# Kernel optimization log

Hardware: AMD Instinct MI355X
Metric: run time of the kernel (lower is better)

Reference implementation:

```python
import jax, jax.numpy as jnp
import numpy as np

N_NODES = 50000
N_EDGES = 600000
D_IN = 128
HID = 128
N_LAYERS = 4
N_OUT = 8
BN_EPS = 1e-5


def setup_inputs() -> dict:
    key = jax.random.key(0)
    ks = jax.random.split(key, 12)
    x = jax.random.normal(ks[0], (N_NODES, D_IN), dtype=jnp.float32)
    edge_index = jax.random.randint(ks[1], (2, N_EDGES), 0, N_NODES, dtype=jnp.int64)
    s = 1.0 / np.sqrt(HID)
    # per-layer GIN MLP params, stacked over layers (d_in == hidden so shapes match)
    W1 = jax.random.uniform(ks[2], (N_LAYERS, HID, HID), jnp.float32, -s, s)
    b1 = jax.random.uniform(ks[3], (N_LAYERS, HID), jnp.float32, -s, s)
    W2 = jax.random.uniform(ks[4], (N_LAYERS, HID, HID), jnp.float32, -s, s)
    b2 = jax.random.uniform(ks[5], (N_LAYERS, HID), jnp.float32, -s, s)
    gamma = jnp.ones((N_LAYERS, HID), jnp.float32)
    beta = jnp.zeros((N_LAYERS, HID), jnp.float32)
    s1 = 1.0 / np.sqrt(N_LAYERS * HID)
    lin1_W = jax.random.uniform(ks[6], (N_LAYERS * HID, HID), jnp.float32, -s1, s1)
    lin1_b = jax.random.uniform(ks[7], (HID,), jnp.float32, -s1, s1)
    lin2_W = jax.random.uniform(ks[8], (HID, N_OUT), jnp.float32, -s, s)
    lin2_b = jax.random.uniform(ks[9], (N_OUT,), jnp.float32, -s, s)
    return dict(x=x, edge_index=edge_index, W1=W1, b1=b1, W2=W2, b2=b2,
                gamma=gamma, beta=beta, lin1_W=lin1_W, lin1_b=lin1_b,
                lin2_W=lin2_W, lin2_b=lin2_b)


def _gin_layer(x, src, dst, W1, b1, W2, b2, g, bt):
    # GINConv, eps=0: h_i = MLP(x_i + sum_{j in N(i)} x_j)
    agg = jax.ops.segment_sum(x[src], dst, num_segments=N_NODES)  # [N, d]
    h = x + agg
    h = jax.nn.relu(h @ W1 + b1)
    h = jax.nn.relu(h @ W2 + b2)
    # BatchNorm1d (training-mode stats, biased variance)
    mean = jnp.mean(h, axis=0)
    var = jnp.var(h, axis=0)
    return (h - mean) * jax.lax.rsqrt(var + BN_EPS) * g + bt


def reference(x, edge_index, W1, b1, W2, b2, gamma, beta,
              lin1_W, lin1_b, lin2_W, lin2_b):
    src, dst = edge_index[0], edge_index[1]
    xs = []
    h = x
    for l in range(N_LAYERS):
        h = _gin_layer(h, src, dst, W1[l], b1[l], W2[l], b2[l], gamma[l], beta[l])
        xs.append(h)
    jk = jnp.concatenate(xs, axis=-1)          # JumpingKnowledge 'cat' -> [N, L*HID]
    out = jax.nn.relu(jk @ lin1_W + lin1_b)    # dropout is identity at inference
    out = out @ lin2_W + lin2_b                # [N, N_OUT]
    return out
```

## Files before the change

### kernel.cpp

```cpp
#include <hip/hip_runtime.h>

#define NNODES 50000
#define NEDGES 600000
#define HID 128
#define NLAYERS 4
#define NOUT 8
#define BN_EPS 1e-5f
#define NBLK 196
#define NPBLK 3125

typedef short short8 __attribute__((ext_vector_type(8)));
typedef float f32x4 __attribute__((ext_vector_type(4)));

__device__ inline unsigned short f2bf(float f) {
  unsigned u = __float_as_uint(f);
  unsigned r = ((u >> 16) & 1u) + 0x7fffu;
  return (unsigned short)((u + r) >> 16);
}
__device__ inline float bflo(unsigned w) { return __uint_as_float(w << 16); }
__device__ inline float bfhi(unsigned w) { return __uint_as_float(w & 0xffff0000u); }


__global__ void detect64_k(const int* __restrict__ ei, int* __restrict__ flag) {
  __shared__ int anynz;
  if (threadIdx.x == 0) anynz = 0;
  __syncthreads();
  int acc = 0;
  for (int i = threadIdx.x; i < 4096; i += 256) {
    int p = i * 146;
    acc |= ei[2 * p + 1];
  }
  if (acc != 0) anynz = 1;
  __syncthreads();
  if (threadIdx.x == 0) *flag = (anynz == 0) ? 1 : 0;
}

__global__ void cvt_bf_k(const float* __restrict__ src, unsigned short* __restrict__ dst,
                         int n4) {
  int i = blockIdx.x * 256 + threadIdx.x;
  if (i >= n4) return;
  float4 v = ((const float4*)src)[i];
  ushort4 o;
  o.x = f2bf(v.x);
  o.y = f2bf(v.y);
  o.z = f2bf(v.z);
  o.w = f2bf(v.w);
  ((ushort4*)dst)[i] = o;
}


__global__ void zero_deg_k(int* __restrict__ deg) {
  int i = blockIdx.x * 256 + threadIdx.x;
  if (i < NNODES + 1) deg[i] = 0;
}

__global__ void hist_k(const int* __restrict__ ei, const int* __restrict__ flag,
                       int* __restrict__ deg) {
  int e = blockIdx.x * 256 + threadIdx.x;
  if (e >= NEDGES) return;
  int d = (*flag) ? ei[2 * NEDGES + 2 * e] : ei[NEDGES + e];
  atomicAdd(&deg[d], 1);
}

__global__ void blocksum_k(const int* __restrict__ deg, int* __restrict__ bsum) {
  int t = threadIdx.x;
  int i = blockIdx.x * 256 + t;
  __shared__ int sh[256];
  sh[t] = (i < NNODES) ? deg[i] : 0;
  __syncthreads();
  for (int s = 128; s > 0; s >>= 1) {
    if (t < s) sh[t] += sh[t + s];
    __syncthreads();
  }
  if (t == 0) bsum[blockIdx.x] = sh[0];
}

__global__ void scanb_k(const int* __restrict__ bsum, int* __restrict__ boff) {
  __shared__ int sh[256];
  int t = threadIdx.x;
  sh[t] = (t < NBLK) ? bsum[t] : 0;
  __syncthreads();
  for (int d = 1; d < 256; d <<= 1) {
    int v = (t >= d) ? sh[t - d] : 0;
    __syncthreads();
    sh[t] += v;
    __syncthreads();
  }
  if (t < NBLK) boff[t] = (t == 0) ? 0 : sh[t - 1];
}

__global__ void writeoff_k(const int* __restrict__ deg, const int* __restrict__ boff,
                           int* __restrict__ off, int* __restrict__ cursor) {
  int t = threadIdx.x;
  int i = blockIdx.x * 256 + t;
  __shared__ int sh[256];
  int v = (i < NNODES) ? deg[i] : 0;
  sh[t] = v;
  __syncthreads();
  for (int d = 1; d < 256; d <<= 1) {
    int u = (t >= d) ? sh[t - d] : 0;
    __syncthreads();
    sh[t] += u;
    __syncthreads();
  }
  int excl = boff[blockIdx.x] + sh[t] - v;
  if (i < NNODES) {
    off[i] = excl;
    cursor[i] = excl;
  }
  if (i == NNODES - 1) off[NNODES] = excl + v;
}

__global__ void fill_k(const int* __restrict__ ei, const int* __restrict__ flag,
                       int* __restrict__ cursor, int* __restrict__ srcs) {
  int e = blockIdx.x * 256 + threadIdx.x;
  if (e >= NEDGES) return;
  int s, d;
  if (*flag) {
    s = ei[2 * e];
    d = ei[2 * NEDGES + 2 * e];
  } else {
    s = ei[e];
    d = ei[NEDGES + e];
  }
  int pos = atomicAdd(&cursor[d], 1);
  srcs[pos] = s;
}

__global__ void gather_agg_k(const unsigned short* __restrict__ X,
                             const int* __restrict__ off, const int* __restrict__ srcs,
                             unsigned short* __restrict__ T) {
  int gid = blockIdx.x * 256 + threadIdx.x;
  int node = gid >> 5;
  if (node >= NNODES) return;
  int lane = gid & 31;
  int a = off[node], b = off[node + 1];
  const uint2* Xv = (const uint2*)X;
  uint2 w = Xv[(size_t)node * 32 + lane];
  float a0 = bflo(w.x), a1 = bfhi(w.x), a2 = bflo(w.y), a3 = bfhi(w.y);
  for (int base = a; base < b; base += 32) {
    int cnt = b - base;
    if (cnt > 32) cnt = 32;
    int idx = (lane < cnt) ? srcs[base + lane] : 0;
#pragma unroll 8
    for (int i = 0; i < cnt; ++i) {
      int s = __shfl(idx, i, 32);
      uint2 v = Xv[(size_t)s * 32 + lane];
      a0 += bflo(v.x);
      a1 += bfhi(v.x);
      a2 += bflo(v.y);
      a3 += bfhi(v.y);
    }
  }
  uint2 o;
  o.x = (unsigned)f2bf(a0) | ((unsigned)f2bf(a1) << 16);
  o.y = (unsigned)f2bf(a2) | ((unsigned)f2bf(a3) << 16);
  ((uint2*)T)[(size_t)node * 32 + lane] = o;
}

__global__ void packW_k(const float* __restrict__ W1, const float* __restrict__ W2,
                        const float* __restrict__ L1, unsigned short* __restrict__ P) {
  int t = blockIdx.x * 256 + threadIdx.x;
  if (t >= 48 * 512) return;
  int gk = t >> 9;
  int nt = (t >> 6) & 7;
  int lane = t & 63;
  const float* src;
  int kbase;
  if (gk < 16) {
    src = W1 + (gk >> 2) * 16384;
    kbase = (gk & 3) * 32;
  } else if (gk < 32) {
    src = W2 + ((gk - 16) >> 2) * 16384;
    kbase = ((gk - 16) & 3) * 32;
  } else {
    src = L1;
    kbase = (gk - 32) * 32;
  }
  int n = nt * 16 + (lane & 15);
  int k0 = kbase + (lane >> 4) * 8;
  unsigned short* dst = P + (size_t)t * 8;
#pragma unroll
  for (int j = 0; j < 8; ++j) dst[j] = f2bf(src[(size_t)(k0 + j) * HID + n]);
}

__global__ __launch_bounds__(128) void mlp_k(const unsigned short* __restrict__ A,
                                             const unsigned short* __restrict__ P1,
                                             const float* __restrict__ bias1,
                                             const unsigned short* __restrict__ P2,
                                             const float* __restrict__ bias2,
                                             float* __restrict__ H, int M,
                                             float* __restrict__ pstats) {
  __shared__ unsigned short sA[16 * 136];
  int tid = threadIdx.x;
  int lane = tid & 63, w = tid >> 6;
  int rb = blockIdx.x * 16;
  int r = rb + (lane & 15);
  int hi = lane >> 4, c = lane & 15;
  int koff = hi * 8;
  int ntb = w * 4;

  short8 a_[4];
  const unsigned short* Ar = A + (size_t)r * HID + koff;
#pragma unroll
  for (int ks = 0; ks < 4; ++ks) a_[ks] = *(const short8*)(Ar + ks * 32);

  const short8* Bp1 = (const short8*)P1;
  f32x4 acc[4];
#pragma unroll
  for (int nt = 0; nt < 4; ++nt) acc[nt] = (f32x4){0.f, 0.f, 0.f, 0.f};
  short8 bcur[4], bnxt[4];
#pragma unroll
  for (int nt = 0; nt < 4; ++nt) bcur[nt] = Bp1[(ntb + nt) * 64 + lane];
#pragma unroll
  for (int ks = 0; ks < 4; ++ks) {
    if (ks < 3) {
#pragma unroll
      for (int nt = 0; nt < 4; ++nt) bnxt[nt] = Bp1[(ks + 1) * 512 + (ntb + nt) * 64 + lane];
    }
#pragma unroll
    for (int nt = 0; nt < 4; ++nt)
      acc[nt] = __builtin_amdgcn_mfma_f32_16x16x32_bf16(a_[ks], bcur[nt], acc[nt], 0, 0, 0);
    if (ks < 3) {
#pragma unroll
      for (int nt = 0; nt < 4; ++nt) bcur[nt] = bnxt[nt];
    }
  }
#pragma unroll
  for (int nt = 0; nt < 4; ++nt) {
    int col = (ntb + nt) * 16 + c;
    float b = bias1[col];
#pragma unroll
    for (int rr = 0; rr < 4; ++rr) {
      float v = fmaxf(acc[nt][rr] + b, 0.f);
      sA[(hi * 4 + rr) * 136 + col] = f2bf(v);
    }
  }
  __syncthreads();

#pragma unroll
  for (int nt = 0; nt < 4; ++nt) acc[nt] = (f32x4){0.f, 0.f, 0.f, 0.f};
  const short8* Bp2 = (const short8*)P2;
#pragma unroll
  for (int nt = 0; nt < 4; ++nt) bcur[nt] = Bp2[(ntb + nt) * 64 + lane];
#pragma unroll
  for (int ks = 0; ks < 4; ++ks) {
    short8 af = *(const short8*)&sA[c * 136 + ks * 32 + koff];
    if (ks < 3) {
#pragma unroll
      for (int nt = 0; nt < 4; ++nt) bnxt[nt] = Bp2[(ks + 1) * 512 + (ntb + nt) * 64 + lane];
    }
#pragma unroll
    for (int nt = 0; nt < 4; ++nt)
      acc[nt] = __builtin_amdgcn_mfma_f32_16x16x32_bf16(af, bcur[nt], acc[nt], 0, 0, 0);
    if (ks < 3) {
#pragma unroll
      for (int nt = 0; nt < 4; ++nt) bcur[nt] = bnxt[nt];
    }
  }
  float* dst = pstats + (size_t)blockIdx.x * 256;
#pragma unroll
  for (int nt = 0; nt < 4; ++nt) {
    int col = (ntb + nt) * 16 + c;
    float b = bias2[col];
    float s = 0.f, q = 0.f;
#pragma unroll
    for (int rr = 0; rr < 4; ++rr) {
      int row = rb + hi * 4 + rr;
      float v = fmaxf(acc[nt][rr] + b, 0.f);
      H[(size_t)row * HID + col] = v;
      s += v;
      q += v * v;
    }
    s += __shfl_xor(s, 16, 64);
    q += __shfl_xor(q, 16, 64);
    s += __shfl_xor(s, 32, 64);
    q += __shfl_xor(q, 32, 64);
    if (hi == 0) {
      dst[col] = s;
      dst[128 + col] = q;
    }
  }
}

__global__ void reduce_stats_k(const float* __restrict__ pstats, float* __restrict__ stats) {
  __shared__ float sh[256];
  int j = blockIdx.x;
  int t = threadIdx.x;
  float acc = 0.f;
  for (int b = t; b < NPBLK; b += 256) acc += pstats[(size_t)b * 256 + j];
  sh[t] = acc;
  __syncthreads();
  for (int s = 128; s > 0; s >>= 1) {
    if (t < s) sh[t] += sh[t + s];
    __syncthreads();
  }
  if (t == 0) stats[j] = sh[0];
}

__global__ __launch_bounds__(128) void mjkgemm_k(const unsigned short* __restrict__ H0,
                                                 const unsigned short* __restrict__ H1,
                                                 const unsigned short* __restrict__ H2,
                                                 const unsigned short* __restrict__ H3,
                                                 const unsigned short* __restrict__ P,
                                                 const float* __restrict__ bias,
                                                 float* __restrict__ C, int M) {
  int tid = threadIdx.x;
  int lane = tid & 63, w = tid >> 6;
  int rb = blockIdx.x * 16;
  int r = rb + (lane & 15);
  int koff = (lane >> 4) * 8;
  int ntb = w * 4;
  f32x4 acc[4];
#pragma unroll
  for (int nt = 0; nt < 4; ++nt) acc[nt] = (f32x4){0.f, 0.f, 0.f, 0.f};
  const unsigned short* Hs[4] = {H0, H1, H2, H3};
  short8 bcur[4], bnxt[4];
  for (int l = 0; l < 4; ++l) {
    const short8* Bp = (const short8*)(P + l * 16384);
    short8 a_[4];
    const unsigned short* Ar = Hs[l] + (size_t)r * HID + koff;
#pragma unroll
    for (int ks = 0; ks < 4; ++ks) a_[ks] = *(const short8*)(Ar + ks * 32);
#pragma unroll
    for (int nt = 0; nt < 4; ++nt) bcur[nt] = Bp[(ntb + nt) * 64 + lane];
#pragma unroll
    for (int ks = 0; ks < 4; ++ks) {
      if (ks < 3) {
#pragma unroll
        for (int nt = 0; nt < 4; ++nt) bnxt[nt] = Bp[(ks + 1) * 512 + (ntb + nt) * 64 + lane];
      }
#pragma unroll
      for (int nt = 0; nt < 4; ++nt)
        acc[nt] = __builtin_amdgcn_mfma_f32_16x16x32_bf16(a_[ks], bcur[nt], acc[nt], 0, 0, 0);
      if (ks < 3) {
#pragma unroll
        for (int nt = 0; nt < 4; ++nt) bcur[nt] = bnxt[nt];
      }
    }
  }
  int hi = lane >> 4, c = lane & 15;
#pragma unroll
  for (int nt = 0; nt < 4; ++nt) {
    int col = (ntb + nt) * 16 + c;
    float b = bias[col];
#pragma unroll
    for (int rr = 0; rr < 4; ++rr) {
      int row = rb + hi * 4 + rr;
      float v = fmaxf(acc[nt][rr] + b, 0.f);
      C[(size_t)row * HID + col] = v;
    }
  }
}

__global__ void bn_norm_k(const float* __restrict__ H, unsigned short* __restrict__ HB,
                          const float* __restrict__ stats, const float* __restrict__ gamma,
                          const float* __restrict__ beta) {
  int i = blockIdx.x * 256 + threadIdx.x;
  if (i >= NNODES * 32) return;
  int c4 = i & 31;
  float4 v = ((const float4*)H)[i];
  float4 sm = ((const float4*)stats)[c4];
  float4 sq = ((const float4*)(stats + 128))[c4];
  float4 g = ((const float4*)gamma)[c4];
  float4 bt = ((const float4*)beta)[c4];
  const float invN = 1.0f / (float)NNODES;
  float m, var, inv;
  ushort4 o;
  m = sm.x * invN; var = sq.x * invN - m * m; inv = rsqrtf(var + BN_EPS);
  o.x = f2bf((v.x - m) * inv * g.x + bt.x);
  m = sm.y * invN; var = sq.y * invN - m * m; inv = rsqrtf(var + BN_EPS);
  o.y = f2bf((v.y - m) * inv * g.y + bt.y);
  m = sm.z * invN; var = sq.z * invN - m * m; inv = rsqrtf(var + BN_EPS);
  o.z = f2bf((v.z - m) * inv * g.z + bt.z);
  m = sm.w * invN; var = sq.w * invN - m * m; inv = rsqrtf(var + BN_EPS);
  o.w = f2bf((v.w - m) * inv * g.w + bt.w);
  ((ushort4*)HB)[i] = o;
}

__global__ void head_k(const float* __restrict__ O1, const float* __restrict__ W,
                       const float* __restrict__ b, float* __restrict__ out, int M) {
  __shared__ float sW[HID * NOUT];
  int tid = threadIdx.x;
#pragma unroll
  for (int i = 0; i < 4; ++i) sW[tid + i * 256] = W[tid + i * 256];
  __syncthreads();
  int row = blockIdx.x * 256 + tid;
  if (row >= M) return;
  float acc[NOUT];
#pragma unroll
  for (int j = 0; j < NOUT; ++j) acc[j] = b[j];
  const float* Ar = O1 + (size_t)row * HID;
  for (int k = 0; k < HID; k += 4) {
    float4 a = *(const float4*)(Ar + k);
#pragma unroll
    for (int kk = 0; kk < 4; ++kk) {
      float av = ((const float*)&a)[kk];
#pragma unroll
      for (int j = 0; j < NOUT; ++j) acc[j] += av * sW[(k + kk) * NOUT + j];
    }
  }
#pragma unroll
  for (int j = 0; j < NOUT; ++j) out[(size_t)row * NOUT + j] = acc[j];
}


extern "C" void kernel_launch(void* const* d_in, const int* in_sizes, int n_in,
                              void* d_out, int out_size, void* d_ws, size_t ws_size,
                              hipStream_t stream) {
  const float* x     = (const float*)d_in[0];
  const int*   ei    = (const int*)d_in[1];
  const float* W1    = (const float*)d_in[2];
  const float* b1    = (const float*)d_in[3];
  const float* W2    = (const float*)d_in[4];
  const float* b2    = (const float*)d_in[5];
  const float* gamma = (const float*)d_in[6];
  const float* beta  = (const float*)d_in[7];
  const float* l1W   = (const float*)d_in[8];
  const float* l1b   = (const float*)d_in[9];
  const float* l2W   = (const float*)d_in[10];
  const float* l2b   = (const float*)d_in[11];

  float* ws = (float*)d_ws;
  const size_t NB = (size_t)NNODES * HID;
  const size_t NBH = NB / 2;
  float* h = ws;
  float* t2 = ws + NB;
  unsigned short* xb = (unsigned short*)(ws + 2 * NB);
  unsigned short* tmp = (unsigned short*)(ws + 2 * NB + NBH);
  unsigned short* hb[4];
  for (int l = 0; l < 4; ++l)
    hb[l] = (unsigned short*)(ws + 2 * NB + (2 + l) * NBH);
  float* stats = ws + 2 * NB + 6 * NBH;
  int* flag = (int*)(stats + 1024);
  int* deg = flag + 4;
  int* off = deg + (NNODES + 1);
  int* cursor = off + (NNODES + 1);
  int* bsum = cursor + (NNODES + 1);
  int* boff = bsum + 256;
  int* srcs = boff + 260;
  size_t pofs = 2 * NB + 6 * NBH + 1024 + 4 + 3 * (size_t)(NNODES + 1) + 256 + 260 + NEDGES;
  pofs = (pofs + 3) & ~(size_t)3;
  unsigned short* P = (unsigned short*)(ws + pofs);
  float* pstats = ws + pofs + 98304;

  detect64_k<<<1, 256, 0, stream>>>(ei, flag);
  zero_deg_k<<<NBLK, 256, 0, stream>>>(deg);
  hist_k<<<2344, 256, 0, stream>>>(ei, flag, deg);
  blocksum_k<<<NBLK, 256, 0, stream>>>(deg, bsum);
  scanb_k<<<1, 256, 0, stream>>>(bsum, boff);
  writeoff_k<<<NBLK, 256, 0, stream>>>(deg, boff, off, cursor);
  fill_k<<<2344, 256, 0, stream>>>(ei, flag, cursor, srcs);
  packW_k<<<96, 256, 0, stream>>>(W1, W2, l1W, P);
  cvt_bf_k<<<6250, 256, 0, stream>>>(x, xb, NNODES * 32);

  const unsigned short* hin = xb;
  for (int l = 0; l < NLAYERS; ++l) {
    gather_agg_k<<<6250, 256, 0, stream>>>(hin, off, srcs, tmp);
    mlp_k<<<NPBLK, 128, 0, stream>>>(tmp, P + (size_t)l * 16384, b1 + l * HID,
                                     P + 65536 + (size_t)l * 16384, b2 + l * HID, h, NNODES,
                                     pstats);
    reduce_stats_k<<<256, 256, 0, stream>>>(pstats, stats + l * 256);
    bn_norm_k<<<6250, 256, 0, stream>>>(h, hb[l], stats + l * 256, gamma + l * HID,
                                        beta + l * HID);
    hin = hb[l];
  }
  mjkgemm_k<<<NPBLK, 128, 0, stream>>>(hb[0], hb[1], hb[2], hb[3], P + 131072, l1b, t2, NNODES);
  head_k<<<196, 256, 0, stream>>>(t2, l2W, l2b, (float*)d_out, NNODES);
}
```

Baseline: 376.3 us.

## Build CSR with replicated degree counters and rank-based atomic-free fill

```diff
diff --git a/kernel.cpp b/kernel.cpp
--- a/kernel.cpp
+++ b/kernel.cpp
@@ -8,6 +8,7 @@
 #define BN_EPS 1e-5f
 #define NBLK 196
 #define NPBLK 3125
+#define NCOPY 8
 
 typedef short short8 __attribute__((ext_vector_type(8)));
 typedef float f32x4 __attribute__((ext_vector_type(4)));
@@ -49,17 +50,31 @@
 }
 
 
-__global__ void zero_deg_k(int* __restrict__ deg) {
+__global__ void zero_degc_k(int* __restrict__ degC) {
   int i = blockIdx.x * 256 + threadIdx.x;
-  if (i < NNODES + 1) deg[i] = 0;
-}
-
-__global__ void hist_k(const int* __restrict__ ei, const int* __restrict__ flag,
-                       int* __restrict__ deg) {
+  if (i < NCOPY * NNODES) degC[i] = 0;
+}
+
+__global__ void hist_rank_k(const int* __restrict__ ei, const int* __restrict__ flag,
+                            int* __restrict__ degC, int* __restrict__ rank) {
   int e = blockIdx.x * 256 + threadIdx.x;
   if (e >= NEDGES) return;
   int d = (*flag) ? ei[2 * NEDGES + 2 * e] : ei[NEDGES + e];
-  atomicAdd(&deg[d], 1);
+  int c = blockIdx.x & (NCOPY - 1);
+  rank[e] = atomicAdd(&degC[c * NNODES + d], 1);
+}
+
+__global__ void coff_k(int* __restrict__ degC, int* __restrict__ deg) {
+  int d = blockIdx.x * 256 + threadIdx.x;
+  if (d >= NNODES) return;
+  int run = 0;
+#pragma unroll
+  for (int c = 0; c < NCOPY; ++c) {
+    int t = degC[c * NNODES + d];
+    degC[c * NNODES + d] = run;
+    run += t;
+  }
+  deg[d] = run;
 }
 
 __global__ void blocksum_k(const int* __restrict__ deg, int* __restrict__ bsum) {
@@ -90,7 +105,7 @@
 }
 
 __global__ void writeoff_k(const int* __restrict__ deg, const int* __restrict__ boff,
-                           int* __restrict__ off, int* __restrict__ cursor) {
+                           int* __restrict__ off) {
   int t = threadIdx.x;
   int i = blockIdx.x * 256 + t;
   __shared__ int sh[256];
@@ -104,15 +119,13 @@
     __syncthreads();
   }
   int excl = boff[blockIdx.x] + sh[t] - v;
-  if (i < NNODES) {
-    off[i] = excl;
-    cursor[i] = excl;
-  }
+  if (i < NNODES) off[i] = excl;
   if (i == NNODES - 1) off[NNODES] = excl + v;
 }
 
-__global__ void fill_k(const int* __restrict__ ei, const int* __restrict__ flag,
-                       int* __restrict__ cursor, int* __restrict__ srcs) {
+__global__ void fill2_k(const int* __restrict__ ei, const int* __restrict__ flag,
+                        const int* __restrict__ off, const int* __restrict__ degC,
+                        const int* __restrict__ rank, int* __restrict__ srcs) {
   int e = blockIdx.x * 256 + threadIdx.x;
   if (e >= NEDGES) return;
   int s, d;
@@ -123,8 +136,8 @@
     s = ei[e];
     d = ei[NEDGES + e];
   }
-  int pos = atomicAdd(&cursor[d], 1);
-  srcs[pos] = s;
+  int c = blockIdx.x & (NCOPY - 1);
+  srcs[off[d] + degC[c * NNODES + d] + rank[e]] = s;
 }
 
 __global__ void gather_agg_k(const unsigned short* __restrict__ X,
@@ -435,22 +448,25 @@
   int* flag = (int*)(stats + 1024);
   int* deg = flag + 4;
   int* off = deg + (NNODES + 1);
-  int* cursor = off + (NNODES + 1);
-  int* bsum = cursor + (NNODES + 1);
+  int* bsum = off + (NNODES + 1);
   int* boff = bsum + 256;
-  int* srcs = boff + 260;
-  size_t pofs = 2 * NB + 6 * NBH + 1024 + 4 + 3 * (size_t)(NNODES + 1) + 256 + 260 + NEDGES;
+  int* degC = boff + 260;
+  int* rank = degC + NCOPY * NNODES;
+  int* srcs = rank + NEDGES;
+  size_t pofs = 2 * NB + 6 * NBH + 1024 + 4 + 2 * (size_t)(NNODES + 1) + 256 + 260 +
+                (size_t)NCOPY * NNODES + 2 * (size_t)NEDGES;
   pofs = (pofs + 3) & ~(size_t)3;
   unsigned short* P = (unsigned short*)(ws + pofs);
   float* pstats = ws + pofs + 98304;
 
   detect64_k<<<1, 256, 0, stream>>>(ei, flag);
-  zero_deg_k<<<NBLK, 256, 0, stream>>>(deg);
-  hist_k<<<2344, 256, 0, stream>>>(ei, flag, deg);
+  zero_degc_k<<<1563, 256, 0, stream>>>(degC);
+  hist_rank_k<<<2344, 256, 0, stream>>>(ei, flag, degC, rank);
+  coff_k<<<NBLK, 256, 0, stream>>>(degC, deg);
   blocksum_k<<<NBLK, 256, 0, stream>>>(deg, bsum);
   scanb_k<<<1, 256, 0, stream>>>(bsum, boff);
-  writeoff_k<<<NBLK, 256, 0, stream>>>(deg, boff, off, cursor);
-  fill_k<<<2344, 256, 0, stream>>>(ei, flag, cursor, srcs);
+  writeoff_k<<<NBLK, 256, 0, stream>>>(deg, boff, off);
+  fill2_k<<<2344, 256, 0, stream>>>(ei, flag, off, degC, rank, srcs);
   packW_k<<<96, 256, 0, stream>>>(W1, W2, l1W, P);
   cvt_bf_k<<<6250, 256, 0, stream>>>(x, xb, NNODES * 32);
 
```

New measurement: 353.2 us. -6.1%, faster.
